# Kernel tuning notes

Hardware: AMD Instinct MI355X
Metric: run time of the kernel (lower is better)

The kernel has to match this reference:

```python
import jax, jax.numpy as jnp
import numpy as np

B, T, N, D, W = 8, 24, 1024, 64, 2
EPS = 1e-5


def setup_inputs() -> dict:
    key = jax.random.key(0)
    ks = jax.random.split(key, 6)
    s = 1.0 / np.sqrt(D)
    x = jax.random.normal(ks[0], (B, T, N, D), dtype=jnp.float32)
    W1 = jax.random.normal(ks[1], (D, D), dtype=jnp.float32) * s
    b1 = jax.random.normal(ks[2], (D,), dtype=jnp.float32) * s
    W2 = jax.random.normal(ks[3], (D, D), dtype=jnp.float32) * s
    b2 = jax.random.normal(ks[4], (D,), dtype=jnp.float32) * s
    gamma = jnp.ones((D,), dtype=jnp.float32)
    beta = jnp.zeros((D,), dtype=jnp.float32)
    # expanded_adj: [N, N*W] = [I | I | ...], then row-normalized (norm_adj ~ D^-1 A)
    adj = jnp.tile(jnp.eye(N, dtype=jnp.float32), (1, W))
    adj = adj / jnp.clip(adj.sum(axis=1, keepdims=True), 1.0, None)
    return {"x": x, "W1": W1, "b1": b1, "W2": W2, "b2": b2,
            "gamma": gamma, "beta": beta, "adj": adj}


def reference(x, W1, b1, W2, b2, gamma, beta, adj):
    Bx, Tx, Nx, Dx = x.shape
    win = adj.shape[1] // Nx
    feat = jnp.pad(x, ((0, 0), (win - 1, 0), (0, 0), (0, 0)))
    g = jnp.stack([feat[:, i:i + Tx] for i in range(win)], axis=2)
    g = g.reshape(Bx, Tx, win * Nx, Dx)
    h1 = jnp.einsum('btmd,ed->btme', g, W1) + b1
    h2 = jnp.einsum('btmd,ed->btme', g, W2) + b2
    a1 = jnp.einsum('nm,btme->btne', adj, h1)  # [B,T,N,D]
    a2 = jnp.einsum('nm,btme->btne', adj, h2)
    full = jax.nn.relu(a1 * a2) + a1
    z = full + x
    mu = z.mean(axis=-1, keepdims=True)
    var = z.var(axis=-1, keepdims=True)
    return (z - mu) * jax.lax.rsqrt(var + EPS) * gamma + beta
```

## Files before the change

kernel.cpp:

```cpp
#include <hip/hip_runtime.h>

#define BB 8
#define TT 24
#define NN 1024
#define DD 64
#define CHAIN 4

typedef float  f32x4  __attribute__((ext_vector_type(4)));
typedef __bf16 bf16x8 __attribute__((ext_vector_type(8)));

__device__ __forceinline__ void gload16(const void* g, void* l) {
    __builtin_amdgcn_global_load_lds(
        (const __attribute__((address_space(1))) void*)g,
        (__attribute__((address_space(3)))       void*)l, 16, 0, 0);
}

__global__ __launch_bounds__(256) void stgcn_kernel(
    const float* __restrict__ x,
    const float* __restrict__ W1,
    const float* __restrict__ b1,
    const float* __restrict__ W2,
    const float* __restrict__ b2,
    const float* __restrict__ gamma,
    const float* __restrict__ beta,
    const float* __restrict__ adj,
    float* __restrict__ out)
{
    const int tid  = threadIdx.x;
    const int lane = tid & 63;
    const int wv   = tid >> 6;
    const int m16  = lane & 15;
    const int quad = lane >> 4;
    const int e4   = quad * 4;

    __shared__ bf16x8 wlds[16][64];
    __shared__ __align__(16) float xbuf[2][4096];
    __shared__ f32x4  plds[4][16];

    for (int s = tid; s < 16 * 64; s += 256) {
        const int g  = s >> 6, l = s & 63;
        const int mat = g >> 3, et = (g >> 1) & 3, ks = g & 1;
        const int ms = l & 15, qs = l >> 4;
        const float* src = (mat ? W2 : W1) + (et * 16 + ms) * DD + ks * 32 + qs * 8;
        const f32x4 a = *(const f32x4*)(src);
        const f32x4 bb = *(const f32x4*)(src + 4);
        bf16x8 f;
#pragma unroll
        for (int j = 0; j < 4; ++j) { f[j] = (__bf16)a[j]; f[j + 4] = (__bf16)bb[j]; }
        wlds[g][l] = f;
    }
    if (tid < 64) {
        const int arr = tid >> 4, j = tid & 15;
        const float* src = (arr == 0) ? b1 : (arr == 1) ? b2 : (arr == 2) ? gamma : beta;
        plds[arr][j] = *(const f32x4*)(src + j * 4);
    }

    const int blk = blockIdx.x;
    const int b   = blk / 96;
    const int rem = blk % 96;
    const int n6  = rem / 6;
    const int tg  = rem % 6;
    const int t0  = tg * CHAIN;
    const int n0  = n6 * 64;

    const int n = n0 + wv * 16 + m16;
    const float c0 = adj[(size_t)n * (NN * 2) + n];
    const float c1 = adj[(size_t)n * (NN * 2) + NN + n];
    const float cb = c0 + c1;
    const float c00 = (t0 > 0) ? c0 : 0.f;

    auto stage = [&](int s, int t) {
        const char* gb = (const char*)(x + ((size_t)(b * TT + t) * NN + n0) * DD);
        char* lb = (char*)&xbuf[s][0];
#pragma unroll
        for (int i = 0; i < 4; ++i) {
            const int D = i * 4096 + tid * 16;
            const int S = D ^ (((D >> 8) & 7) << 4);
            gload16(gb + S, lb + D);
        }
    };

    stage(0, (t0 > 0) ? t0 - 1 : t0);
    stage(1, t0);
    __syncthreads();

    const int R   = wv * 16 + m16;
    const int RB  = R * 256;
    const int SW  = (m16 & 7) << 4;
    const int q32 = quad * 32;

#pragma unroll
    for (int k = 0; k < CHAIN; ++k) {
        const int t = t0 + k;
        const float c0k = (k == 0) ? c00 : c0;
        const char* cbuf = (const char*)&xbuf[(k & 1) ^ 1][0];
        const char* pbuf = (const char*)&xbuf[k & 1][0];

        const f32x4 cc0 = *(const f32x4*)(cbuf + ((RB + q32      ) ^ SW));
        const f32x4 cc1 = *(const f32x4*)(cbuf + ((RB + q32 + 16 ) ^ SW));
        const f32x4 cc2 = *(const f32x4*)(cbuf + ((RB + 128 + q32) ^ SW));
        const f32x4 cc3 = *(const f32x4*)(cbuf + ((RB + 144 + q32) ^ SW));
        const f32x4 pp0 = *(const f32x4*)(pbuf + ((RB + q32      ) ^ SW));
        const f32x4 pp1 = *(const f32x4*)(pbuf + ((RB + q32 + 16 ) ^ SW));
        const f32x4 pp2 = *(const f32x4*)(pbuf + ((RB + 128 + q32) ^ SW));
        const f32x4 pp3 = *(const f32x4*)(pbuf + ((RB + 144 + q32) ^ SW));
        f32x4 xe[4];
#pragma unroll
        for (int et = 0; et < 4; ++et)
            xe[et] = *(const f32x4*)(cbuf + ((RB + et * 64 + quad * 16) ^ SW));

        __syncthreads();
        if (k + 1 < CHAIN) stage(k & 1, t + 1);

        bf16x8 X0, X1;
#pragma unroll
        for (int j = 0; j < 4; ++j) {
            X0[j]     = (__bf16)(c0k * pp0[j] + c1 * cc0[j]);
            X0[j + 4] = (__bf16)(c0k * pp1[j] + c1 * cc1[j]);
            X1[j]     = (__bf16)(c0k * pp2[j] + c1 * cc2[j]);
            X1[j + 4] = (__bf16)(c0k * pp3[j] + c1 * cc3[j]);
        }

        f32x4 acc1[4], acc2[4];
#pragma unroll
        for (int et = 0; et < 4; ++et) {
            acc1[et] = (f32x4){0.f, 0.f, 0.f, 0.f};
            acc2[et] = (f32x4){0.f, 0.f, 0.f, 0.f};
        }
#pragma unroll
        for (int et = 0; et < 4; ++et) {
            const bf16x8 w10 = wlds[et * 2 + 0][lane];
            const bf16x8 w11 = wlds[et * 2 + 1][lane];
            const bf16x8 w20 = wlds[8 + et * 2 + 0][lane];
            const bf16x8 w21 = wlds[8 + et * 2 + 1][lane];
            acc1[et] = __builtin_amdgcn_mfma_f32_16x16x32_bf16(w10, X0, acc1[et], 0, 0, 0);
            acc1[et] = __builtin_amdgcn_mfma_f32_16x16x32_bf16(w11, X1, acc1[et], 0, 0, 0);
            acc2[et] = __builtin_amdgcn_mfma_f32_16x16x32_bf16(w20, X0, acc2[et], 0, 0, 0);
            acc2[et] = __builtin_amdgcn_mfma_f32_16x16x32_bf16(w21, X1, acc2[et], 0, 0, 0);
        }

        float s = 0.f, s2 = 0.f;
#pragma unroll
        for (int et = 0; et < 4; ++et) {
            const f32x4 b1v = plds[0][et * 4 + quad];
            const f32x4 b2v = plds[1][et * 4 + quad];
#pragma unroll
            for (int r = 0; r < 4; ++r) {
                const float A1v = acc1[et][r] + cb * b1v[r];
                const float A2v = acc2[et][r] + cb * b2v[r];
                const float p   = A1v * A2v;
                const float full = (p > 0.f ? p : 0.f) + A1v;
                const float zz = full + xe[et][r];
                acc1[et][r] = zz;
                s  += zz;
                s2 += zz * zz;
            }
        }

        s  += __shfl_xor(s, 16, 64);
        s2 += __shfl_xor(s2, 16, 64);
        s  += __shfl_xor(s, 32, 64);
        s2 += __shfl_xor(s2, 32, 64);

        const float mu  = s * (1.f / 64.f);
        const float var = s2 * (1.f / 64.f) - mu * mu;
        const float rs  = rsqrtf(var + 1e-5f);

        float* orow = out + ((size_t)(b * TT + t) * NN + n0 + R) * DD;
#pragma unroll
        for (int et = 0; et < 4; ++et) {
            const f32x4 gvv = plds[2][et * 4 + quad];
            const f32x4 bev = plds[3][et * 4 + quad];
            f32x4 o;
#pragma unroll
            for (int r = 0; r < 4; ++r)
                o[r] = (acc1[et][r] - mu) * rs * gvv[r] + bev[r];
            *(f32x4*)(orow + et * 16 + e4) = o;
        }

        if (k + 1 < CHAIN) __syncthreads();
    }
}

extern "C" void kernel_launch(void* const* d_in, const int* in_sizes, int n_in,
                              void* d_out, int out_size, void* d_ws, size_t ws_size,
                              hipStream_t stream) {
    const float* x     = (const float*)d_in[0];
    const float* W1    = (const float*)d_in[1];
    const float* b1    = (const float*)d_in[2];
    const float* W2    = (const float*)d_in[3];
    const float* b2    = (const float*)d_in[4];
    const float* gamma = (const float*)d_in[5];
    const float* beta  = (const float*)d_in[6];
    const float* adj   = (const float*)d_in[7];
    float* out = (float*)d_out;

    dim3 grid(768), block(256);
    hipLaunchKernelGGL(stgcn_kernel, grid, block, 0, stream,
                       x, W1, b1, W2, b2, gamma, beta, adj, out);
}
```

Measured before the change: 119.3 us.

## Replace LDS-staged time chain with direct global loads, one timestep per wave

Drops the double-buffered global-to-LDS staging and the 4-timestep chain per block. Each wave now handles 16 nodes at one timestep and loads its current and previous rows straight from global memory into registers, with the grid enlarged from 768 to 3072 blocks. This removes LDS traffic and block-wide barriers and raises parallelism. In exchange, the previous-timestep rows are read twice from global memory (hopefully from cache), and the W/bias setup runs four times as often.

```diff
diff --git a/kernel.cpp b/kernel.cpp
--- a/kernel.cpp
+++ b/kernel.cpp
@@ -4,16 +4,9 @@
 #define TT 24
 #define NN 1024
 #define DD 64
-#define CHAIN 4
 
 typedef float  f32x4  __attribute__((ext_vector_type(4)));
 typedef __bf16 bf16x8 __attribute__((ext_vector_type(8)));
-
-__device__ __forceinline__ void gload16(const void* g, void* l) {
-    __builtin_amdgcn_global_load_lds(
-        (const __attribute__((address_space(1))) void*)g,
-        (__attribute__((address_space(3)))       void*)l, 16, 0, 0);
-}
 
 __global__ __launch_bounds__(256) void stgcn_kernel(
     const float* __restrict__ x,
@@ -32,9 +25,9 @@
     const int m16  = lane & 15;
     const int quad = lane >> 4;
     const int e4   = quad * 4;
+    const int q8   = quad * 8;
 
     __shared__ bf16x8 wlds[16][64];
-    __shared__ __align__(16) float xbuf[2][4096];
     __shared__ f32x4  plds[4][16];
 
     for (int s = tid; s < 16 * 64; s += 256) {
@@ -42,7 +35,7 @@
         const int mat = g >> 3, et = (g >> 1) & 3, ks = g & 1;
         const int ms = l & 15, qs = l >> 4;
         const float* src = (mat ? W2 : W1) + (et * 16 + ms) * DD + ks * 32 + qs * 8;
-        const f32x4 a = *(const f32x4*)(src);
+        const f32x4 a  = *(const f32x4*)(src);
         const f32x4 bb = *(const f32x4*)(src + 4);
         bf16x8 f;
 #pragma unroll
@@ -54,131 +47,101 @@
         const float* src = (arr == 0) ? b1 : (arr == 1) ? b2 : (arr == 2) ? gamma : beta;
         plds[arr][j] = *(const f32x4*)(src + j * 4);
     }
+    __syncthreads();
 
-    const int blk = blockIdx.x;
-    const int b   = blk / 96;
-    const int rem = blk % 96;
-    const int n6  = rem / 6;
-    const int tg  = rem % 6;
-    const int t0  = tg * CHAIN;
-    const int n0  = n6 * 64;
+    const int wid = blockIdx.x * 4 + wv;
+    const int t   = (wid >> 6) % TT;
+    const int n   = (wid & 63) * 16 + m16;
 
-    const int n = n0 + wv * 16 + m16;
     const float c0 = adj[(size_t)n * (NN * 2) + n];
     const float c1 = adj[(size_t)n * (NN * 2) + NN + n];
     const float cb = c0 + c1;
-    const float c00 = (t0 > 0) ? c0 : 0.f;
+    const float c0d = (t > 0) ? c0 : 0.f;
+    const ptrdiff_t poff = (t > 0) ? -(ptrdiff_t)(NN * DD) : 0;
 
-    auto stage = [&](int s, int t) {
-        const char* gb = (const char*)(x + ((size_t)(b * TT + t) * NN + n0) * DD);
-        char* lb = (char*)&xbuf[s][0];
+    const float* xr = x + ((size_t)wid * 16 + m16) * DD;
+    const float* xq = xr + poff;
+
+    const f32x4 cc0 = *(const f32x4*)(xr + q8);
+    const f32x4 cc1 = *(const f32x4*)(xr + q8 + 4);
+    const f32x4 cc2 = *(const f32x4*)(xr + 32 + q8);
+    const f32x4 cc3 = *(const f32x4*)(xr + 36 + q8);
+    const f32x4 pp0 = *(const f32x4*)(xq + q8);
+    const f32x4 pp1 = *(const f32x4*)(xq + q8 + 4);
+    const f32x4 pp2 = *(const f32x4*)(xq + 32 + q8);
+    const f32x4 pp3 = *(const f32x4*)(xq + 36 + q8);
+
+    bf16x8 X0, X1;
 #pragma unroll
-        for (int i = 0; i < 4; ++i) {
-            const int D = i * 4096 + tid * 16;
-            const int S = D ^ (((D >> 8) & 7) << 4);
-            gload16(gb + S, lb + D);
+    for (int j = 0; j < 4; ++j) {
+        X0[j]     = (__bf16)(c0d * pp0[j] + c1 * cc0[j]);
+        X0[j + 4] = (__bf16)(c0d * pp1[j] + c1 * cc1[j]);
+        X1[j]     = (__bf16)(c0d * pp2[j] + c1 * cc2[j]);
+        X1[j + 4] = (__bf16)(c0d * pp3[j] + c1 * cc3[j]);
+    }
+
+    f32x4 acc1[4], acc2[4];
+#pragma unroll
+    for (int et = 0; et < 4; ++et) {
+        acc1[et] = (f32x4){0.f, 0.f, 0.f, 0.f};
+        acc2[et] = (f32x4){0.f, 0.f, 0.f, 0.f};
+    }
+#pragma unroll
+    for (int et = 0; et < 4; ++et) {
+        const bf16x8 w10 = wlds[et * 2 + 0][lane];
+        const bf16x8 w11 = wlds[et * 2 + 1][lane];
+        const bf16x8 w20 = wlds[8 + et * 2 + 0][lane];
+        const bf16x8 w21 = wlds[8 + et * 2 + 1][lane];
+        acc1[et] = __builtin_amdgcn_mfma_f32_16x16x32_bf16(w10, X0, acc1[et], 0, 0, 0);
+        acc1[et] = __builtin_amdgcn_mfma_f32_16x16x32_bf16(w11, X1, acc1[et], 0, 0, 0);
+        acc2[et] = __builtin_amdgcn_mfma_f32_16x16x32_bf16(w20, X0, acc2[et], 0, 0, 0);
+        acc2[et] = __builtin_amdgcn_mfma_f32_16x16x32_bf16(w21, X1, acc2[et], 0, 0, 0);
+    }
+
+    __builtin_amdgcn_sched_barrier(0);
+
+    f32x4 xe[4];
+#pragma unroll
+    for (int et = 0; et < 4; ++et)
+        xe[et] = *(const f32x4*)(xr + et * 16 + e4);
+
+    float s = 0.f, s2 = 0.f;
+#pragma unroll
+    for (int et = 0; et < 4; ++et) {
+        const f32x4 b1v = plds[0][et * 4 + quad];
+        const f32x4 b2v = plds[1][et * 4 + quad];
+#pragma unroll
+        for (int r = 0; r < 4; ++r) {
+            const float A1v = acc1[et][r] + cb * b1v[r];
+            const float A2v = acc2[et][r] + cb * b2v[r];
+            const float p   = A1v * A2v;
+            const float full = (p > 0.f ? p : 0.f) + A1v;
+            const float zz = full + xe[et][r];
+            acc1[et][r] = zz;
+            s  += zz;
+            s2 += zz * zz;
         }
-    };
+    }
 
-    stage(0, (t0 > 0) ? t0 - 1 : t0);
-    stage(1, t0);
-    __syncthreads();
+    s  += __shfl_xor(s, 16, 64);
+    s2 += __shfl_xor(s2, 16, 64);
+    s  += __shfl_xor(s, 32, 64);
+    s2 += __shfl_xor(s2, 32, 64);
 
-    const int R   = wv * 16 + m16;
-    const int RB  = R * 256;
-    const int SW  = (m16 & 7) << 4;
-    const int q32 = quad * 32;
+    const float mu  = s * (1.f / 64.f);
+    const float var = s2 * (1.f / 64.f) - mu * mu;
+    const float rs  = rsqrtf(var + 1e-5f);
 
+    float* orow = out + ((size_t)wid * 16 + m16) * DD;
 #pragma unroll
-    for (int k = 0; k < CHAIN; ++k) {
-        const int t = t0 + k;
-        const float c0k = (k == 0) ? c00 : c0;
-        const char* cbuf = (const char*)&xbuf[(k & 1) ^ 1][0];
-        const char* pbuf = (const char*)&xbuf[k & 1][0];
-
-        const f32x4 cc0 = *(const f32x4*)(cbuf + ((RB + q32      ) ^ SW));
-        const f32x4 cc1 = *(const f32x4*)(cbuf + ((RB + q32 + 16 ) ^ SW));
-        const f32x4 cc2 = *(const f32x4*)(cbuf + ((RB + 128 + q32) ^ SW));
-        const f32x4 cc3 = *(const f32x4*)(cbuf + ((RB + 144 + q32) ^ SW));
-        const f32x4 pp0 = *(const f32x4*)(pbuf + ((RB + q32      ) ^ SW));
-        const f32x4 pp1 = *(const f32x4*)(pbuf + ((RB + q32 + 16 ) ^ SW));
-        const f32x4 pp2 = *(const f32x4*)(pbuf + ((RB + 128 + q32) ^ SW));
-        const f32x4 pp3 = *(const f32x4*)(pbuf + ((RB + 144 + q32) ^ SW));
-        f32x4 xe[4];
+    for (int et = 0; et < 4; ++et) {
+        const f32x4 gvv = plds[2][et * 4 + quad];
+        const f32x4 bev = plds[3][et * 4 + quad];
+        f32x4 o;
 #pragma unroll
-        for (int et = 0; et < 4; ++et)
-            xe[et] = *(const f32x4*)(cbuf + ((RB + et * 64 + quad * 16) ^ SW));
-
-        __syncthreads();
-        if (k + 1 < CHAIN) stage(k & 1, t + 1);
-
-        bf16x8 X0, X1;
-#pragma unroll
-        for (int j = 0; j < 4; ++j) {
-            X0[j]     = (__bf16)(c0k * pp0[j] + c1 * cc0[j]);
-            X0[j + 4] = (__bf16)(c0k * pp1[j] + c1 * cc1[j]);
-            X1[j]     = (__bf16)(c0k * pp2[j] + c1 * cc2[j]);
-            X1[j + 4] = (__bf16)(c0k * pp3[j] + c1 * cc3[j]);
-        }
-
-        f32x4 acc1[4], acc2[4];
-#pragma unroll
-        for (int et = 0; et < 4; ++et) {
-            acc1[et] = (f32x4){0.f, 0.f, 0.f, 0.f};
-            acc2[et] = (f32x4){0.f, 0.f, 0.f, 0.f};
-        }
-#pragma unroll
-        for (int et = 0; et < 4; ++et) {
-            const bf16x8 w10 = wlds[et * 2 + 0][lane];
-            const bf16x8 w11 = wlds[et * 2 + 1][lane];
-            const bf16x8 w20 = wlds[8 + et * 2 + 0][lane];
-            const bf16x8 w21 = wlds[8 + et * 2 + 1][lane];
-            acc1[et] = __builtin_amdgcn_mfma_f32_16x16x32_bf16(w10, X0, acc1[et], 0, 0, 0);
-            acc1[et] = __builtin_amdgcn_mfma_f32_16x16x32_bf16(w11, X1, acc1[et], 0, 0, 0);
-            acc2[et] = __builtin_amdgcn_mfma_f32_16x16x32_bf16(w20, X0, acc2[et], 0, 0, 0);
-            acc2[et] = __builtin_amdgcn_mfma_f32_16x16x32_bf16(w21, X1, acc2[et], 0, 0, 0);
-        }
-
-        float s = 0.f, s2 = 0.f;
-#pragma unroll
-        for (int et = 0; et < 4; ++et) {
-            const f32x4 b1v = plds[0][et * 4 + quad];
-            const f32x4 b2v = plds[1][et * 4 + quad];
-#pragma unroll
-            for (int r = 0; r < 4; ++r) {
-                const float A1v = acc1[et][r] + cb * b1v[r];
-                const float A2v = acc2[et][r] + cb * b2v[r];
-                const float p   = A1v * A2v;
-                const float full = (p > 0.f ? p : 0.f) + A1v;
-                const float zz = full + xe[et][r];
-                acc1[et][r] = zz;
-                s  += zz;
-                s2 += zz * zz;
-            }
-        }
-
-        s  += __shfl_xor(s, 16, 64);
-        s2 += __shfl_xor(s2, 16, 64);
-        s  += __shfl_xor(s, 32, 64);
-        s2 += __shfl_xor(s2, 32, 64);
-
-        const float mu  = s * (1.f / 64.f);
-        const float var = s2 * (1.f / 64.f) - mu * mu;
-        const float rs  = rsqrtf(var + 1e-5f);
-
-        float* orow = out + ((size_t)(b * TT + t) * NN + n0 + R) * DD;
-#pragma unroll
-        for (int et = 0; et < 4; ++et) {
-            const f32x4 gvv = plds[2][et * 4 + quad];
-            const f32x4 bev = plds[3][et * 4 + quad];
-            f32x4 o;
-#pragma unroll
-            for (int r = 0; r < 4; ++r)
-                o[r] = (acc1[et][r] - mu) * rs * gvv[r] + bev[r];
-            *(f32x4*)(orow + et * 16 + e4) = o;
-        }
-
-        if (k + 1 < CHAIN) __syncthreads();
+        for (int r = 0; r < 4; ++r)
+            o[r] = (acc1[et][r] - mu) * rs * gvv[r] + bev[r];
+        *(f32x4*)(orow + et * 16 + e4) = o;
     }
 }
 
@@ -195,7 +158,7 @@
     const float* adj   = (const float*)d_in[7];
     float* out = (float*)d_out;
 
-    dim3 grid(768), block(256);
+    dim3 grid(3072), block(256);
     hipLaunchKernelGGL(stgcn_kernel, grid, block, 0, stream,
                        x, W1, b1, W2, b2, gamma, beta, adj, out);
 }
```

After: 129.2 us. +8.3%, slower.
